# Optimization experiments

Measured on AMD Instinct MI355X. Metric: run time of the kernel, lower is better.

The kernel has to match this reference:

```python
import jax, jax.numpy as jnp
import numpy as np

INPUT_SIZE = 350   # (133 + 42) * 2
HIDDEN = 2048

def setup_inputs() -> dict:
    key = jax.random.key(0)
    ks = jax.random.split(key, 11)
    s = 0.02
    H4 = 4 * HIDDEN
    return {
        "x":     jax.random.normal(ks[0], (1, 133, 2), jnp.float32),
        "W_ih0": jax.random.normal(ks[1], (H4, INPUT_SIZE), jnp.float32) * s,
        "W_hh0": jax.random.normal(ks[2], (H4, HIDDEN), jnp.float32) * s,
        "b_ih0": jax.random.normal(ks[3], (H4,), jnp.float32) * s,
        "b_hh0": jax.random.normal(ks[4], (H4,), jnp.float32) * s,
        "W_ih1": jax.random.normal(ks[5], (H4, HIDDEN), jnp.float32) * s,
        "W_hh1": jax.random.normal(ks[6], (H4, HIDDEN), jnp.float32) * s,
        "b_ih1": jax.random.normal(ks[7], (H4,), jnp.float32) * s,
        "b_hh1": jax.random.normal(ks[8], (H4,), jnp.float32) * s,
        "fc_w":  jax.random.normal(ks[9], (INPUT_SIZE, HIDDEN), jnp.float32) * s,
        "fc_b":  jax.random.normal(ks[10], (INPUT_SIZE,), jnp.float32) * s,
    }

def _prepare(x):
    kp = x[0].astype(jnp.float32)                 # [133, 2]
    src_body, src_face = kp[0], kp[53]
    src_left, src_right = kp[100], kp[121]
    body = kp[:17] - src_body
    feet = kp[17:23]                              # never recentered in original
    face = kp[23:91] - src_face
    l0, r0 = kp[91:112], kp[112:133]
    # bounding-box scales computed BEFORE recentering (matches torch order)
    wl = l0[:, 0].max() - l0[:, 0].min(); hl = l0[:, 1].max() - l0[:, 1].min()
    wr = r0[:, 0].max() - r0[:, 0].min(); hr = r0[:, 1].max() - r0[:, 1].min()
    chin2l = l0 - src_body
    chin2r = r0 - src_body
    left = l0 - src_left
    right = r0 - src_right
    okl = (wl != 0.0) & (hl != 0.0)
    okr = (wr != 0.0) & (hr != 0.0)
    dl = jnp.where(okl, jnp.stack([wl, hl]), jnp.ones(2, kp.dtype))
    dr = jnp.where(okr, jnp.stack([wr, hr]), jnp.ones(2, kp.dtype))
    left = left / dl
    right = right / dr
    return jnp.concatenate([body, feet, face, left, right, chin2l, chin2r]).reshape(INPUT_SIZE)

def _lstm_cell(xin, h, c, Wih, Whh, bih, bhh):
    g = Wih @ xin + bih + Whh @ h + bhh           # [4H]
    i, f, gg, o = jnp.split(g, 4)                 # PyTorch gate order i,f,g,o
    c_new = jax.nn.sigmoid(f) * c + jax.nn.sigmoid(i) * jnp.tanh(gg)
    h_new = jax.nn.sigmoid(o) * jnp.tanh(c_new)
    return h_new, c_new

def reference(x, W_ih0, W_hh0, b_ih0, b_hh0, W_ih1, W_hh1, b_ih1, b_hh1, fc_w, fc_b):
    feat = _prepare(x)                            # [350]
    h0 = jnp.zeros(HIDDEN, feat.dtype)            # initialize_cell_and_hidden_state
    c0 = jnp.zeros(HIDDEN, feat.dtype)
    h1, _ = _lstm_cell(feat, h0, c0, W_ih0, W_hh0, b_ih0, b_hh0)
    h2, _ = _lstm_cell(h1, h0, c0, W_ih1, W_hh1, b_ih1, b_hh1)
    return (fc_w @ h2 + fc_b)[None, :]            # [1, 350]
```

## Files before the change

### kernel.cpp

```cpp
#include <hip/hip_runtime.h>
#include <math.h>

#define HIDDEN 2048
#define IN_F 350

__device__ __forceinline__ float sigmoidf_(float v) { return 1.0f / (1.0f + expf(-v)); }
__device__ __forceinline__ float dot4_(float4 a, float4 b) {
    return a.x*b.x + a.y*b.y + a.z*b.z + a.w*b.w;
}

__global__ __launch_bounds__(768) void k1_feat_lstm0(
    const float* __restrict__ x, const float* __restrict__ Wih,
    const float* __restrict__ bih, const float* __restrict__ bhh,
    float* __restrict__ h1)
{
    __shared__ __align__(16) float feat[IN_F];
    __shared__ float hx[84];
    __shared__ float sc[12];
    __shared__ float ext[4];
    __shared__ float gd[12];
    const int tid = threadIdx.x, wave = tid >> 6, lane = tid & 63;
    const int b = blockIdx.x;

    if (tid < 84) hx[tid] = x[182 + tid];
    else if (tid < 92) {
        int t = tid - 84;
        int p = t >> 1;
        int base = (p == 0) ? 0 : (p == 1) ? 106 : (p == 2) ? 200 : 242;
        sc[t] = x[base + (t & 1)];
    }
    __syncthreads();
    if (tid < 4) {
        const int h = tid >> 1, c = tid & 1;
        float m = hx[h*42 + c], M = m;
        #pragma unroll
        for (int jj = 1; jj < 21; ++jj) {
            float v = hx[h*42 + 2*jj + c];
            m = fminf(m, v); M = fmaxf(M, v);
        }
        ext[tid] = M - m;
    }
    __syncthreads();
    if (tid < 4) {
        const int h = tid >> 1;
        bool ok = (ext[2*h] != 0.0f) && (ext[2*h + 1] != 0.0f);
        sc[8 + tid] = ok ? ext[tid] : 1.0f;
    }
    __syncthreads();
    if (tid < 133) {
        const float sbx = sc[0], sby = sc[1], sfx = sc[2], sfy = sc[3];
        const float slx = sc[4], sly = sc[5], srx = sc[6], sry = sc[7];
        const float dlx = sc[8], dly = sc[9], drx = sc[10], dry = sc[11];
        const int k = tid;
        float vx = x[2*k], vy = x[2*k + 1];
        if (k < 17) {
            feat[2*k]   = vx - sbx;  feat[2*k+1] = vy - sby;
        } else if (k < 23) {
            feat[2*k]   = vx;        feat[2*k+1] = vy;
        } else if (k < 91) {
            feat[2*k]   = vx - sfx;  feat[2*k+1] = vy - sfy;
        } else if (k < 112) {
            int jj = k - 91;
            feat[182 + 2*jj] = (vx - slx) / dlx;  feat[183 + 2*jj] = (vy - sly) / dly;
            feat[266 + 2*jj] = vx - sbx;          feat[267 + 2*jj] = vy - sby;
        } else {
            int jj = k - 112;
            feat[224 + 2*jj] = (vx - srx) / drx;  feat[225 + 2*jj] = (vy - sry) / dry;
            feat[308 + 2*jj] = vx - sbx;          feat[309 + 2*jj] = vy - sby;
        }
    }
    __syncthreads();

    const int u = b * 4 + wave / 3;
    const int gate = wave % 3;
    const int grow = ((gate == 0) ? 0 : (gate == 1) ? 2 : 3) * HIDDEN + u;
    const float2* wr = (const float2*)(Wih + (size_t)grow * IN_F);
    const float2* f2 = (const float2*)feat;
    const bool has2 = (128 + lane) < 175;
    float2 w0 = wr[lane];
    float2 w1 = wr[64 + lane];
    float2 w2 = has2 ? wr[128 + lane] : make_float2(0.f, 0.f);
    float2 f0 = f2[lane];
    float2 f1 = f2[64 + lane];
    float2 fx = has2 ? f2[128 + lane] : make_float2(0.f, 0.f);
    float acc = w0.x*f0.x + w0.y*f0.y + w1.x*f1.x + w1.y*f1.y + w2.x*fx.x + w2.y*fx.y;
    #pragma unroll
    for (int off = 32; off; off >>= 1) acc += __shfl_down(acc, off);
    if (lane == 0) gd[wave] = acc + bih[grow] + bhh[grow];
    __syncthreads();
    if (tid < 4) {
        float c = sigmoidf_(gd[3*tid + 0]) * tanhf(gd[3*tid + 1]);
        h1[b*4 + tid] = sigmoidf_(gd[3*tid + 2]) * tanhf(c);
    }
}

__global__ __launch_bounds__(384) void k2_lstm1(
    const float* __restrict__ Wih, const float* __restrict__ bih,
    const float* __restrict__ bhh, const float* __restrict__ h1,
    float* __restrict__ h2)
{
    __shared__ __align__(16) float h1s[HIDDEN];
    __shared__ float gd[6];
    const int tid = threadIdx.x, wave = tid >> 6, lane = tid & 63;
    const int b = blockIdx.x;

    {
        const float4* h4g = (const float4*)h1;
        float4* h4s = (float4*)h1s;
        h4s[tid] = h4g[tid];
        if (tid < 128) h4s[384 + tid] = h4g[384 + tid];
    }
    __syncthreads();

    const int u = b * 2 + (wave >= 3 ? 1 : 0);
    const int gate = wave % 3;
    const int grow = ((gate == 0) ? 0 : (gate == 1) ? 2 : 3) * HIDDEN + u;
    const float4* wr = (const float4*)(Wih + (size_t)grow * HIDDEN);
    const float4* h4 = (const float4*)h1s;

    float4 wv0 = wr[lane];
    float4 wv1 = wr[ 64 + lane];
    float4 wv2 = wr[128 + lane];
    float4 wv3 = wr[192 + lane];
    float4 wv4 = wr[256 + lane];
    float4 wv5 = wr[320 + lane];
    float4 wv6 = wr[384 + lane];
    float4 wv7 = wr[448 + lane];

    float acc = dot4_(wv0, h4[lane])       + dot4_(wv1, h4[ 64 + lane])
              + dot4_(wv2, h4[128 + lane]) + dot4_(wv3, h4[192 + lane])
              + dot4_(wv4, h4[256 + lane]) + dot4_(wv5, h4[320 + lane])
              + dot4_(wv6, h4[384 + lane]) + dot4_(wv7, h4[448 + lane]);
    #pragma unroll
    for (int off = 32; off; off >>= 1) acc += __shfl_down(acc, off);
    if (lane == 0) gd[wave] = acc + bih[grow] + bhh[grow];
    __syncthreads();
    if (tid < 2) {
        float c = sigmoidf_(gd[3*tid + 0]) * tanhf(gd[3*tid + 1]);
        h2[b*2 + tid] = sigmoidf_(gd[3*tid + 2]) * tanhf(c);
    }
}

__global__ __launch_bounds__(256) void k3_fc(
    const float* __restrict__ h2, const float* __restrict__ W,
    const float* __restrict__ b, float* __restrict__ out)
{
    __shared__ float part[4];
    const int tid = threadIdx.x, wave = tid >> 6, lane = tid & 63;
    const int r = blockIdx.x;
    const float4* wr = (const float4*)(W + (size_t)r * HIDDEN);
    const float4* h4 = (const float4*)h2;
    const int base = wave * 128;
    float4 w0 = wr[base + lane], w1 = wr[base + 64 + lane];
    float4 v0 = h4[base + lane], v1 = h4[base + 64 + lane];
    float acc = dot4_(w0, v0) + dot4_(w1, v1);
    #pragma unroll
    for (int off = 32; off; off >>= 1) acc += __shfl_down(acc, off);
    if (lane == 0) part[wave] = acc;
    __syncthreads();
    if (tid == 0) out[r] = part[0] + part[1] + part[2] + part[3] + b[r];
}

extern "C" void kernel_launch(void* const* d_in, const int* in_sizes, int n_in,
                              void* d_out, int out_size, void* d_ws, size_t ws_size,
                              hipStream_t stream) {
    const float* x     = (const float*)d_in[0];
    const float* W_ih0 = (const float*)d_in[1];
    const float* b_ih0 = (const float*)d_in[3];
    const float* b_hh0 = (const float*)d_in[4];
    const float* W_ih1 = (const float*)d_in[5];
    const float* b_ih1 = (const float*)d_in[7];
    const float* b_hh1 = (const float*)d_in[8];
    const float* fc_w  = (const float*)d_in[9];
    const float* fc_b  = (const float*)d_in[10];

    float* h1 = (float*)d_ws;
    float* h2 = (float*)d_ws + HIDDEN;

    k1_feat_lstm0<<<512, 768, 0, stream>>>(x, W_ih0, b_ih0, b_hh0, h1);
    k2_lstm1<<<1024, 384, 0, stream>>>(W_ih1, b_ih1, b_hh1, h1, h2);
    k3_fc<<<IN_F, 256, 0, stream>>>(h2, fc_w, fc_b, (float*)d_out);
}
```

Before: 22.29 us.

## Fuse FC layer into LSTM1 kernel via atomic partial sums

Removes the separate FC kernel. Each block of the layer-1 kernel now computes 4 hidden units instead of 2, keeps them in shared memory, and atomically adds its 4-column contribution to every output. The output is pre-seeded with the FC bias inside the first kernel. This saves one launch and the h2 round trip through global memory. In exchange it adds 350 atomics per block and strided, uncoalesced 16-byte reads of fc_w, and float summation order becomes nondeterministic.

```diff
diff --git a/kernel.cpp b/kernel.cpp
--- a/kernel.cpp
+++ b/kernel.cpp
@@ -12,7 +12,8 @@
 __global__ __launch_bounds__(768) void k1_feat_lstm0(
     const float* __restrict__ x, const float* __restrict__ Wih,
     const float* __restrict__ bih, const float* __restrict__ bhh,
-    float* __restrict__ h1)
+    const float* __restrict__ fcb, float* __restrict__ h1,
+    float* __restrict__ out)
 {
     __shared__ __align__(16) float feat[IN_F];
     __shared__ float hx[84];
@@ -22,9 +23,11 @@
     const int tid = threadIdx.x, wave = tid >> 6, lane = tid & 63;
     const int b = blockIdx.x;
 
+    if (b < IN_F && tid == 767) out[b] = fcb[b];
+
     if (tid < 84) hx[tid] = x[182 + tid];
-    else if (tid < 92) {
-        int t = tid - 84;
+    else if (tid >= 128 && tid < 136) {
+        int t = tid - 128;
         int p = t >> 1;
         int base = (p == 0) ? 0 : (p == 1) ? 106 : (p == 2) ? 200 : 242;
         sc[t] = x[base + (t & 1)];
@@ -94,25 +97,25 @@
     }
 }
 
-__global__ __launch_bounds__(384) void k2_lstm1(
+__global__ __launch_bounds__(768) void k2_lstm1_fc(
     const float* __restrict__ Wih, const float* __restrict__ bih,
-    const float* __restrict__ bhh, const float* __restrict__ h1,
-    float* __restrict__ h2)
+    const float* __restrict__ bhh, const float* __restrict__ fcw,
+    const float* __restrict__ h1, float* __restrict__ out)
 {
     __shared__ __align__(16) float h1s[HIDDEN];
-    __shared__ float gd[6];
+    __shared__ float gd[12];
+    __shared__ __align__(16) float h2s[4];
     const int tid = threadIdx.x, wave = tid >> 6, lane = tid & 63;
     const int b = blockIdx.x;
 
     {
         const float4* h4g = (const float4*)h1;
         float4* h4s = (float4*)h1s;
-        h4s[tid] = h4g[tid];
-        if (tid < 128) h4s[384 + tid] = h4g[384 + tid];
+        if (tid < 512) h4s[tid] = h4g[tid];
     }
     __syncthreads();
 
-    const int u = b * 2 + (wave >= 3 ? 1 : 0);
+    const int u = b * 4 + wave / 3;
     const int gate = wave % 3;
     const int grow = ((gate == 0) ? 0 : (gate == 1) ? 2 : 3) * HIDDEN + u;
     const float4* wr = (const float4*)(Wih + (size_t)grow * HIDDEN);
@@ -135,30 +138,17 @@
     for (int off = 32; off; off >>= 1) acc += __shfl_down(acc, off);
     if (lane == 0) gd[wave] = acc + bih[grow] + bhh[grow];
     __syncthreads();
-    if (tid < 2) {
+    if (tid < 4) {
         float c = sigmoidf_(gd[3*tid + 0]) * tanhf(gd[3*tid + 1]);
-        h2[b*2 + tid] = sigmoidf_(gd[3*tid + 2]) * tanhf(c);
+        h2s[tid] = sigmoidf_(gd[3*tid + 2]) * tanhf(c);
     }
-}
+    __syncthreads();
 
-__global__ __launch_bounds__(256) void k3_fc(
-    const float* __restrict__ h2, const float* __restrict__ W,
-    const float* __restrict__ b, float* __restrict__ out)
-{
-    __shared__ float part[4];
-    const int tid = threadIdx.x, wave = tid >> 6, lane = tid & 63;
-    const int r = blockIdx.x;
-    const float4* wr = (const float4*)(W + (size_t)r * HIDDEN);
-    const float4* h4 = (const float4*)h2;
-    const int base = wave * 128;
-    float4 w0 = wr[base + lane], w1 = wr[base + 64 + lane];
-    float4 v0 = h4[base + lane], v1 = h4[base + 64 + lane];
-    float acc = dot4_(w0, v0) + dot4_(w1, v1);
-    #pragma unroll
-    for (int off = 32; off; off >>= 1) acc += __shfl_down(acc, off);
-    if (lane == 0) part[wave] = acc;
-    __syncthreads();
-    if (tid == 0) out[r] = part[0] + part[1] + part[2] + part[3] + b[r];
+    if (tid < IN_F) {
+        float4 w = *(const float4*)(fcw + (size_t)tid * HIDDEN + b * 4);
+        float4 h2v = *(const float4*)h2s;
+        atomicAdd(&out[tid], dot4_(w, h2v));
+    }
 }
 
 extern "C" void kernel_launch(void* const* d_in, const int* in_sizes, int n_in,
@@ -175,9 +165,9 @@
     const float* fc_b  = (const float*)d_in[10];
 
     float* h1 = (float*)d_ws;
-    float* h2 = (float*)d_ws + HIDDEN;
 
-    k1_feat_lstm0<<<512, 768, 0, stream>>>(x, W_ih0, b_ih0, b_hh0, h1);
-    k2_lstm1<<<1024, 384, 0, stream>>>(W_ih1, b_ih1, b_hh1, h1, h2);
-    k3_fc<<<IN_F, 256, 0, stream>>>(h2, fc_w, fc_b, (float*)d_out);
+    k1_feat_lstm0<<<512, 768, 0, stream>>>(x, W_ih0, b_ih0, b_hh0, fc_b, h1,
+                                           (float*)d_out);
+    k2_lstm1_fc<<<512, 768, 0, stream>>>(W_ih1, b_ih1, b_hh1, fc_w, h1,
+                                         (float*)d_out);
 }
```

Result: slower. 30.36 us (+36.2%).

## Split layer-1 gate rows across waves and fuse cell nonlinearity into FC kernel

Applied to the files above, without the earlier changes.

The layer-1 kernel now computes one gate row per wave, with four independent rows per block. It reads h1 straight from global memory instead of staging it in shared memory, and it no longer needs a block barrier. The LSTM cell nonlinearity moves into the FC kernel, where each block recomputes all 2048 h2 values from the stored gate pre-activations before its dot product. This removes the shared-memory staging and barrier from the weight-streaming kernel. In exchange, every one of the 350 FC blocks redundantly reads 6144 gate values and evaluates the transcendentals. There is also a minor change to which threads load the scale coordinates in k1.

```diff
diff --git a/kernel.cpp b/kernel.cpp
--- a/kernel.cpp
+++ b/kernel.cpp
@@ -3,6 +3,7 @@
 
 #define HIDDEN 2048
 #define IN_F 350
+
 
 __device__ __forceinline__ float sigmoidf_(float v) { return 1.0f / (1.0f + expf(-v)); }
 __device__ __forceinline__ float dot4_(float4 a, float4 b) {
@@ -23,8 +24,8 @@
     const int b = blockIdx.x;
 
     if (tid < 84) hx[tid] = x[182 + tid];
-    else if (tid < 92) {
-        int t = tid - 84;
+    else if (tid >= 128 && tid < 136) {
+        int t = tid - 128;
         int p = t >> 1;
         int base = (p == 0) ? 0 : (p == 1) ? 106 : (p == 2) ? 200 : 242;
         sc[t] = x[base + (t & 1)];
@@ -94,71 +95,63 @@
     }
 }
 
-__global__ __launch_bounds__(384) void k2_lstm1(
+__global__ __launch_bounds__(256) void k2_rows(
     const float* __restrict__ Wih, const float* __restrict__ bih,
     const float* __restrict__ bhh, const float* __restrict__ h1,
-    float* __restrict__ h2)
+    float* __restrict__ gates)
 {
-    __shared__ __align__(16) float h1s[HIDDEN];
-    __shared__ float gd[6];
+    const int wave = threadIdx.x >> 6, lane = threadIdx.x & 63;
+    const int row = blockIdx.x * 4 + wave;
+    const int g = row >> 11;
+    const int j = row & (HIDDEN - 1);
+    const int grow = ((g == 0) ? 0 : (g == 1) ? 2 : 3) * HIDDEN + j;
+    const float4* wr = (const float4*)(Wih + (size_t)grow * HIDDEN);
+    const float4* h4 = (const float4*)h1;
+
+    float4 w0 = wr[lane],       w1 = wr[ 64 + lane];
+    float4 w2 = wr[128 + lane], w3 = wr[192 + lane];
+    float4 w4 = wr[256 + lane], w5 = wr[320 + lane];
+    float4 w6 = wr[384 + lane], w7 = wr[448 + lane];
+
+    float acc = dot4_(w0, h4[lane])       + dot4_(w1, h4[ 64 + lane])
+              + dot4_(w2, h4[128 + lane]) + dot4_(w3, h4[192 + lane])
+              + dot4_(w4, h4[256 + lane]) + dot4_(w5, h4[320 + lane])
+              + dot4_(w6, h4[384 + lane]) + dot4_(w7, h4[448 + lane]);
+    #pragma unroll
+    for (int off = 32; off; off >>= 1) acc += __shfl_down(acc, off);
+    if (lane == 0) gates[row] = acc + bih[grow] + bhh[grow];
+}
+
+__global__ __launch_bounds__(256) void k3_fc(
+    const float* __restrict__ gates, const float* __restrict__ fcw,
+    const float* __restrict__ fcb, float* __restrict__ out)
+{
+    __shared__ __align__(16) float h2s[HIDDEN];
+    __shared__ float part[4];
     const int tid = threadIdx.x, wave = tid >> 6, lane = tid & 63;
-    const int b = blockIdx.x;
+    const int r = blockIdx.x;
 
-    {
-        const float4* h4g = (const float4*)h1;
-        float4* h4s = (float4*)h1s;
-        h4s[tid] = h4g[tid];
-        if (tid < 128) h4s[384 + tid] = h4g[384 + tid];
+    #pragma unroll
+    for (int it = 0; it < HIDDEN / 256; ++it) {
+        const int j = it * 256 + tid;
+        float gi = gates[j];
+        float gg = gates[HIDDEN + j];
+        float go = gates[2 * HIDDEN + j];
+        float c = sigmoidf_(gi) * tanhf(gg);
+        h2s[j] = sigmoidf_(go) * tanhf(c);
     }
     __syncthreads();
 
-    const int u = b * 2 + (wave >= 3 ? 1 : 0);
-    const int gate = wave % 3;
-    const int grow = ((gate == 0) ? 0 : (gate == 1) ? 2 : 3) * HIDDEN + u;
-    const float4* wr = (const float4*)(Wih + (size_t)grow * HIDDEN);
-    const float4* h4 = (const float4*)h1s;
-
-    float4 wv0 = wr[lane];
-    float4 wv1 = wr[ 64 + lane];
-    float4 wv2 = wr[128 + lane];
-    float4 wv3 = wr[192 + lane];
-    float4 wv4 = wr[256 + lane];
-    float4 wv5 = wr[320 + lane];
-    float4 wv6 = wr[384 + lane];
-    float4 wv7 = wr[448 + lane];
-
-    float acc = dot4_(wv0, h4[lane])       + dot4_(wv1, h4[ 64 + lane])
-              + dot4_(wv2, h4[128 + lane]) + dot4_(wv3, h4[192 + lane])
-              + dot4_(wv4, h4[256 + lane]) + dot4_(wv5, h4[320 + lane])
-              + dot4_(wv6, h4[384 + lane]) + dot4_(wv7, h4[448 + lane]);
-    #pragma unroll
-    for (int off = 32; off; off >>= 1) acc += __shfl_down(acc, off);
-    if (lane == 0) gd[wave] = acc + bih[grow] + bhh[grow];
-    __syncthreads();
-    if (tid < 2) {
-        float c = sigmoidf_(gd[3*tid + 0]) * tanhf(gd[3*tid + 1]);
-        h2[b*2 + tid] = sigmoidf_(gd[3*tid + 2]) * tanhf(c);
-    }
-}
-
-__global__ __launch_bounds__(256) void k3_fc(
-    const float* __restrict__ h2, const float* __restrict__ W,
-    const float* __restrict__ b, float* __restrict__ out)
-{
-    __shared__ float part[4];
-    const int tid = threadIdx.x, wave = tid >> 6, lane = tid & 63;
-    const int r = blockIdx.x;
-    const float4* wr = (const float4*)(W + (size_t)r * HIDDEN);
-    const float4* h4 = (const float4*)h2;
+    const float4* wr = (const float4*)(fcw + (size_t)r * HIDDEN);
+    const float4* h4 = (const float4*)h2s;
     const int base = wave * 128;
-    float4 w0 = wr[base + lane], w1 = wr[base + 64 + lane];
-    float4 v0 = h4[base + lane], v1 = h4[base + 64 + lane];
-    float acc = dot4_(w0, v0) + dot4_(w1, v1);
+    float acc = dot4_(wr[base + lane], h4[base + lane])
+              + dot4_(wr[base + 64 + lane], h4[base + 64 + lane]);
     #pragma unroll
     for (int off = 32; off; off >>= 1) acc += __shfl_down(acc, off);
     if (lane == 0) part[wave] = acc;
     __syncthreads();
-    if (tid == 0) out[r] = part[0] + part[1] + part[2] + part[3] + b[r];
+    if (tid == 0) out[r] = part[0] + part[1] + part[2] + part[3] + fcb[r];
 }
 
 extern "C" void kernel_launch(void* const* d_in, const int* in_sizes, int n_in,
@@ -174,10 +167,10 @@
     const float* fc_w  = (const float*)d_in[9];
     const float* fc_b  = (const float*)d_in[10];
 
-    float* h1 = (float*)d_ws;
-    float* h2 = (float*)d_ws + HIDDEN;
+    float* h1    = (float*)d_ws;
+    float* gates = (float*)d_ws + HIDDEN;
 
     k1_feat_lstm0<<<512, 768, 0, stream>>>(x, W_ih0, b_ih0, b_hh0, h1);
-    k2_lstm1<<<1024, 384, 0, stream>>>(W_ih1, b_ih1, b_hh1, h1, h2);
-    k3_fc<<<IN_F, 256, 0, stream>>>(h2, fc_w, fc_b, (float*)d_out);
+    k2_rows<<<6144 / 4, 256, 0, stream>>>(W_ih1, b_ih1, b_hh1, h1, gates);
+    k3_fc<<<IN_F, 256, 0, stream>>>(gates, fc_w, fc_b, (float*)d_out);
 }
```

New measurement: 25.62 us. 14.9% more time.
